# Kernel optimization log

Hardware: AMD Instinct MI355X
Metric: run time of the kernel (lower is better)

## Reference

```python
import jax, jax.numpy as jnp
import numpy as np

LENS = 0.4
DECAY = 0.2
THRESH = 0.2
LOG_SIG_MIN, LOG_SIG_MAX = -20.0, 2.0

# Surrogate-gradient spike: forward is heaviside, backward is rectangular window |x|<lens
@jax.custom_vjp
def act_fun(x):
    return (x > 0.0).astype(x.dtype)

def _act_fwd(x):
    return act_fun(x), x

def _act_bwd(x, g):
    return (g * (jnp.abs(x) < LENS).astype(g.dtype),)

act_fun.defvjp(_act_fwd, _act_bwd)


def _xavier(k, shape):
    fan_out, fan_in = shape
    lim = float(np.sqrt(6.0 / (fan_in + fan_out)))
    return jax.random.uniform(k, shape, jnp.float32, -lim, lim)


def setup_inputs() -> dict:
    key = jax.random.key(0)
    ks = jax.random.split(key, 9)
    B, IN, H, A = 4096, 512, 2048, 32
    return {
        "state": jax.random.normal(ks[0], (B, 5, IN), jnp.float32),
        "W_lif": _xavier(ks[1], (H, IN)), "b_lif": jnp.zeros((H,), jnp.float32),
        "W11": _xavier(ks[2], (H, H)), "b11": jnp.zeros((H,), jnp.float32),
        "W12": _xavier(ks[3], (H, H)), "b12": jnp.zeros((H,), jnp.float32),
        "W21": _xavier(ks[4], (H, H)), "b21": jnp.zeros((H,), jnp.float32),
        "W22": _xavier(ks[5], (H, H)), "b22": jnp.zeros((H,), jnp.float32),
        "Wm": _xavier(ks[6], (A, H)), "bm": jnp.zeros((A,), jnp.float32),
        "Wls": _xavier(ks[7], (A, H)), "bls": jnp.zeros((A,), jnp.float32),
    }


def reference(state, W_lif, b_lif, W11, b11, W12, b12, W21, b21, W22, b22, Wm, bm, Wls, bls):
    x_seq = jnp.repeat(state, 3, axis=1)
    # precompute fc(x) for all steps in one GEMM: [B,15,H]
    fc = jnp.einsum('bti,hi->bth', x_seq, W_lif) + b_lif
    B, T, H = fc.shape

    def step(carry, fc_t):
        mem, spike = carry
        mem1 = mem * DECAY * (1.0 - spike) + fc_t
        spike1 = act_fun(mem1 - THRESH)
        return (mem1, spike1), spike1

    init = (jnp.zeros((B, H), fc.dtype), jnp.zeros((B, H), fc.dtype))
    _, spikes = jax.lax.scan(step, init, jnp.swapaxes(fc, 0, 1))  # [T,B,H]
    x = jnp.mean(spikes, axis=0)  # [B,H]

    x1 = jax.nn.relu(x @ W11.T + b11)
    x1 = jax.nn.relu(x1 @ W12.T + b12)
    mean = x1 @ Wm.T + bm

    x2 = jax.nn.relu(x @ W21.T + b21)
    x2 = jax.nn.relu(x2 @ W22.T + b22)
    log_std = jnp.clip(x2 @ Wls.T + bls, LOG_SIG_MIN, LOG_SIG_MAX)
    return mean, log_std
```

## Files before the change

### kernel.cpp

```cpp
#include <hip/hip_runtime.h>
#include <hip/hip_bf16.h>


typedef _Float16 f16;
using f32x4 = __attribute__((ext_vector_type(4))) float;
using f16x8 = __attribute__((ext_vector_type(8))) f16;

#define MFMA16(a, b, c) __builtin_amdgcn_mfma_f32_16x16x32_f16((a), (b), (c), 0, 0, 0)
#define VMW8()  asm volatile("s_waitcnt vmcnt(8)" ::: "memory")
#define VMW4()  asm volatile("s_waitcnt vmcnt(4)" ::: "memory")
#define VMW0()  asm volatile("s_waitcnt vmcnt(0)" ::: "memory")
#define LGKM0() asm volatile("s_waitcnt lgkmcnt(0)" ::: "memory")
#define BARRIER() __builtin_amdgcn_s_barrier()
#define SCHED0() __builtin_amdgcn_sched_barrier(0)

__device__ __forceinline__ void gload16(const void* g, void* l) {
  __builtin_amdgcn_global_load_lds(
      (const __attribute__((address_space(1))) unsigned int*)g,
      (__attribute__((address_space(3))) unsigned int*)l, 16, 0, 0);
}

__device__ __forceinline__ void cvt8(const float4& a, const float4& b, f16* dst) {
  f16x8 d;
  d[0] = (f16)a.x; d[1] = (f16)a.y; d[2] = (f16)a.z; d[3] = (f16)a.w;
  d[4] = (f16)b.x; d[5] = (f16)b.y; d[6] = (f16)b.z; d[7] = (f16)b.w;
  *(f16x8*)dst = d;
}

__global__ __launch_bounds__(256) void cvt2b_kernel(
    const float* __restrict__ s0, f16* __restrict__ d0, int n8a,
    const float* __restrict__ s1, f16* __restrict__ d1, int n8b)
{
  int i = blockIdx.x * 256 + threadIdx.x;
  const float* src; f16* dst; int k;
  if (i < n8a) { src = s0; dst = d0; k = i; }
  else { k = i - n8a; if (k >= n8b) return; src = s1; dst = d1; }
  const float4* s4 = (const float4*)src;
  float4 a = s4[(size_t)k * 2], b = s4[(size_t)k * 2 + 1];
  cvt8(a, b, dst + (size_t)k * 8);
}

__global__ __launch_bounds__(256) void cvt4_kernel(
    const float* __restrict__ w0, const float* __restrict__ w1,
    const float* __restrict__ w2, const float* __restrict__ w3,
    f16* __restrict__ dst)
{
  int i = blockIdx.x * 256 + threadIdx.x;
  int which = i >> 19, k = i & 524287;
  const float* src = (which == 0) ? w0 : (which == 1) ? w1 : (which == 2) ? w2 : w3;
  const float4* s4 = (const float4*)src;
  float4 a = s4[(size_t)k * 2], b = s4[(size_t)k * 2 + 1];
  cvt8(a, b, dst + (size_t)i * 8);
}

__global__ __launch_bounds__(256) void cvt2_kernel(
    const float* __restrict__ s0, const float* __restrict__ s1,
    f16* __restrict__ d0, f16* __restrict__ d1, int n8each)
{
  int i = blockIdx.x * 256 + threadIdx.x;
  const float* src = (i < n8each) ? s0 : s1;
  f16* dst = (i < n8each) ? d0 : d1;
  int k = (i < n8each) ? i : i - n8each;
  if (k >= n8each) return;
  const float4* s4 = (const float4*)src;
  float4 a = s4[(size_t)k * 2], b = s4[(size_t)k * 2 + 1];
  cvt8(a, b, dst + (size_t)k * 8);
}

__global__ __launch_bounds__(512, 1) void lif256_kernel(
    const f16* __restrict__ S,
    const f16* __restrict__ W,
    const float* __restrict__ bl,
    f16* __restrict__ X)
{
  __shared__ alignas(16) f16 lds[4][128 * 64];

  const int tid = threadIdx.x, wid = tid >> 6, lane = tid & 63;
  const int wg = ((int)blockIdx.x % 8) * 64 + (int)blockIdx.x / 8;
  const int bn = wg & 15, bm = wg >> 4;
  const int b0 = bm * 128, h0 = bn * 128;
  const int wr0 = (wid >> 2) * 64, wc0 = (wid & 3) * 32;
  const int fr = lane & 15, fq = lane >> 4;
  const int sr = tid >> 3, scb = (tid & 7) * 16;

  f32x4 acc[4][2] = {};
  float mem[4][2][4] = {};
  float cnt[4][2][4] = {};

  char* Lb = (char*)&lds[0][0];
  const int xsw = (fr & 7) << 4;
  const int x0 = (fq * 16) ^ xsw;
  const int x1 = (64 + fq * 16) ^ xsw;
  char* const pA0 = Lb + (wr0 + fr) * 128 + x0;
  char* const pA1 = Lb + (wr0 + fr) * 128 + x1;
  char* const pB0 = Lb + 32768 + (wc0 + fr) * 128 + x0;
  char* const pB1 = Lb + 32768 + (wc0 + fr) * 128 + x1;

  const f16* sBase[2]; const f16* wBase[2];
#pragma unroll
  for (int l = 0; l < 2; ++l) {
    const int row = l * 64 + sr;
    const int c2 = scb ^ ((row & 7) << 4);
    sBase[l] = S + (size_t)(b0 + row) * 2560 + (c2 >> 1);
    wBase[l] = W + (size_t)(h0 + row) * 512 + (c2 >> 1);
  }

  auto STAGE = [&](int slot, int g) {
    const int koff = (g >> 3) * 512 + (g & 7) * 64;
    const int kw = (g & 7) * 64;
#pragma unroll
    for (int l = 0; l < 2; ++l)
      gload16(sBase[l] + koff, Lb + slot * 16384 + l * 8192 + tid * 16);
#pragma unroll
    for (int l = 0; l < 2; ++l)
      gload16(wBase[l] + kw, Lb + 32768 + slot * 16384 + l * 8192 + tid * 16);
  };

  const float bias[2] = { bl[h0 + wc0 + fr], bl[h0 + wc0 + 16 + fr] };

  STAGE(0, 0);
  STAGE(1, 1);
  VMW4();
  BARRIER();
  SCHED0();

#pragma unroll 2
  for (int g = 0; g < 40; ++g) {
    const int slot = g & 1;
    const int so = slot * 16384;

    f16x8 b[2][2], a[2][2];
#pragma unroll
    for (int nf = 0; nf < 2; ++nf) {
      b[nf][0] = *(const f16x8*)(pB0 + so + nf * 2048);
      b[nf][1] = *(const f16x8*)(pB1 + so + nf * 2048);
    }
#pragma unroll
    for (int i = 0; i < 2; ++i) {
      a[i][0] = *(const f16x8*)(pA0 + so + i * 2048);
      a[i][1] = *(const f16x8*)(pA1 + so + i * 2048);
    }
    BARRIER(); LGKM0(); SCHED0();
    __builtin_amdgcn_s_setprio(1);
#pragma unroll
    for (int i = 0; i < 2; ++i)
#pragma unroll
      for (int nf = 0; nf < 2; ++nf) {
        acc[i][nf] = MFMA16(a[i][0], b[nf][0], acc[i][nf]);
        acc[i][nf] = MFMA16(a[i][1], b[nf][1], acc[i][nf]);
      }
    __builtin_amdgcn_s_setprio(0);
    BARRIER();

#pragma unroll
    for (int i = 0; i < 2; ++i) {
      a[i][0] = *(const f16x8*)(pA0 + so + (2 + i) * 2048);
      a[i][1] = *(const f16x8*)(pA1 + so + (2 + i) * 2048);
    }
    LGKM0(); SCHED0();
    BARRIER();
    if (g + 2 < 40) STAGE(slot, g + 2);
    SCHED0();
    __builtin_amdgcn_s_setprio(1);
#pragma unroll
    for (int i = 0; i < 2; ++i)
#pragma unroll
      for (int nf = 0; nf < 2; ++nf) {
        acc[2 + i][nf] = MFMA16(a[i][0], b[nf][0], acc[2 + i][nf]);
        acc[2 + i][nf] = MFMA16(a[i][1], b[nf][1], acc[2 + i][nf]);
      }
    __builtin_amdgcn_s_setprio(0);

    if ((g & 7) == 7) {
#pragma unroll
      for (int mf = 0; mf < 4; ++mf)
#pragma unroll
        for (int nf = 0; nf < 2; ++nf) {
#pragma unroll
          for (int r = 0; r < 4; ++r) {
            const float fc = acc[mf][nf][r] + bias[nf];
            float m = mem[mf][nf][r], c = cnt[mf][nf][r];
#pragma unroll
            for (int j = 0; j < 3; ++j) {
              m = ((m > 0.2f) ? 0.f : m * 0.2f) + fc;
              c += (m > 0.2f) ? 1.f : 0.f;
            }
            mem[mf][nf][r] = m; cnt[mf][nf][r] = c;
          }
          acc[mf][nf] = f32x4{0.f, 0.f, 0.f, 0.f};
        }
    }

    if (g + 2 < 40)      { VMW4(); }
    else if (g + 1 < 40) { VMW0(); }
    BARRIER();
    SCHED0();
  }

#pragma unroll
  for (int nf = 0; nf < 2; ++nf) {
    const int col = h0 + wc0 + nf * 16 + fr;
#pragma unroll
    for (int mf = 0; mf < 4; ++mf) {
      const int row0 = b0 + wr0 + mf * 16 + fq * 4;
#pragma unroll
      for (int r = 0; r < 4; ++r)
        X[(size_t)(row0 + r) * 2048 + col] = (f16)(cnt[mf][nf][r] / 15.0f);
    }
  }
}

__global__ __launch_bounds__(512, 2) void trunk256_kernel(
    const f16* __restrict__ A0, const f16* __restrict__ A1, int lda,
    const f16* __restrict__ W0, const f16* __restrict__ W1,
    const float* __restrict__ bb0, const float* __restrict__ bb1,
    f16* __restrict__ C0, f16* __restrict__ C1, int ldc,
    int nbm, int nbn_half, int K)
{
  __shared__ alignas(16) f16 lds[4][256 * 64];

  const int tid = threadIdx.x, wid = tid >> 6, lane = tid & 63;
  const int nwg = nbm * nbn_half * 2, q8 = nwg / 8;
  const int wg = ((int)blockIdx.x % 8) * q8 + (int)blockIdx.x / 8;
  const int bmi = wg % nbm, t = wg / nbm;
  const int half = (t >= nbn_half);
  const f16* Ap = half ? A1 : A0;
  const f16* Wp = half ? W1 : W0;
  const float* bias = half ? bb1 : bb0;
  f16* C = half ? C1 : C0;
  const int bm0 = bmi * 256;
  const int bn0 = (half ? t - nbn_half : t) * 256;

  const int wr0 = (wid >> 2) * 128, wc0 = (wid & 3) * 64;
  const int fr = lane & 15, fq = lane >> 4;
  const int sr = tid >> 3, scb = (tid & 7) * 16;

  f32x4 acc[8][4] = {};
  const int NT = K / 64;

  char* Lb = (char*)&lds[0][0];
  const int xsw = (fr & 7) << 4;
  const int x0 = (fq * 16) ^ xsw;
  const int x1 = (64 + fq * 16) ^ xsw;
  char* const pA0 = Lb + (wr0 + fr) * 128 + x0;
  char* const pA1 = Lb + (wr0 + fr) * 128 + x1;
  char* const pB0 = Lb + 65536 + (wc0 + fr) * 128 + x0;
  char* const pB1 = Lb + 65536 + (wc0 + fr) * 128 + x1;

  const f16* aBase[4]; const f16* wBase[4];
#pragma unroll
  for (int l = 0; l < 4; ++l) {
    const int row = l * 64 + sr;
    const int c2 = scb ^ ((row & 7) << 4);
    aBase[l] = Ap + (size_t)(bm0 + row) * lda + (c2 >> 1);
    wBase[l] = Wp + (size_t)(bn0 + row) * K + (c2 >> 1);
  }

  auto STAGE = [&](int slot, int kt) {
    const int koff = kt * 64;
#pragma unroll
    for (int l = 0; l < 4; ++l)
      gload16(aBase[l] + koff, Lb + slot * 32768 + l * 8192 + tid * 16);
#pragma unroll
    for (int l = 0; l < 4; ++l)
      gload16(wBase[l] + koff, Lb + 65536 + slot * 32768 + l * 8192 + tid * 16);
  };

  STAGE(0, 0);
  STAGE(1, 1);
  VMW8();
  BARRIER();
  SCHED0();

#pragma unroll 2
  for (int kt = 0; kt < NT; ++kt) {
    const int slot = kt & 1;
    const int so = slot * 32768;

    f16x8 b[4][2];
#pragma unroll
    for (int nf = 0; nf < 4; ++nf) {
      b[nf][0] = *(const f16x8*)(pB0 + so + nf * 2048);
      b[nf][1] = *(const f16x8*)(pB1 + so + nf * 2048);
    }
    f16x8 a0[2][2], a1[2][2];
#pragma unroll
    for (int i = 0; i < 2; ++i) {
      a0[i][0] = *(const f16x8*)(pA0 + so + i * 2048);
      a0[i][1] = *(const f16x8*)(pA1 + so + i * 2048);
    }

    auto QUAD = [&](int mbase, f16x8 (&a)[2][2]) {
      __builtin_amdgcn_s_setprio(1);
#pragma unroll
      for (int nf = 0; nf < 4; ++nf) {
        acc[mbase][nf]     = MFMA16(a[0][0], b[nf][0], acc[mbase][nf]);
        acc[mbase][nf]     = MFMA16(a[0][1], b[nf][1], acc[mbase][nf]);
        acc[mbase + 1][nf] = MFMA16(a[1][0], b[nf][0], acc[mbase + 1][nf]);
        acc[mbase + 1][nf] = MFMA16(a[1][1], b[nf][1], acc[mbase + 1][nf]);
      }
      __builtin_amdgcn_s_setprio(0);
    };

#pragma unroll
    for (int i = 0; i < 2; ++i) {
      a1[i][0] = *(const f16x8*)(pA0 + so + (2 + i) * 2048);
      a1[i][1] = *(const f16x8*)(pA1 + so + (2 + i) * 2048);
    }
    QUAD(0, a0);
#pragma unroll
    for (int i = 0; i < 2; ++i) {
      a0[i][0] = *(const f16x8*)(pA0 + so + (4 + i) * 2048);
      a0[i][1] = *(const f16x8*)(pA1 + so + (4 + i) * 2048);
    }
    QUAD(2, a1);
#pragma unroll
    for (int i = 0; i < 2; ++i) {
      a1[i][0] = *(const f16x8*)(pA0 + so + (6 + i) * 2048);
      a1[i][1] = *(const f16x8*)(pA1 + so + (6 + i) * 2048);
    }
    QUAD(4, a0);
    QUAD(6, a1);

    LGKM0();
    BARRIER();
    SCHED0();
    if (kt + 2 < NT) {
      STAGE(slot, kt + 2);
      SCHED0();
      VMW8();
    } else if (kt + 1 < NT) {
      VMW0();
    }
    BARRIER();
    SCHED0();
  }

#pragma unroll
  for (int nf = 0; nf < 4; ++nf) {
    const int col = bn0 + wc0 + nf * 16 + fr;
    const float bv = bias[col];
#pragma unroll
    for (int m = 0; m < 8; ++m) {
      const int row0 = bm0 + wr0 + m * 16 + fq * 4;
#pragma unroll
      for (int r = 0; r < 4; ++r) {
        float v = fmaxf(acc[m][nf][r] + bv, 0.f);
        C[(size_t)(row0 + r) * ldc + col] = (f16)v;
      }
    }
  }
}

__global__ __launch_bounds__(256) void head_kernel(
    const f16* __restrict__ H1, const f16* __restrict__ H2,
    const f16* __restrict__ Wm, const float* __restrict__ bm,
    const f16* __restrict__ Wls, const float* __restrict__ bls,
    float* __restrict__ OUT, int M, int K)
{
  const int tid = threadIdx.x, wid = tid >> 6, lane = tid & 63;
  const int m0 = blockIdx.x * 64 + wid * 16;
  const int kb = (lane >> 4) * 8, fr = lane & 15, fq = lane >> 4;

  f32x4 a1[2] = {}, a2[2] = {};
  for (int k0 = 0; k0 < K; k0 += 32) {
    f16x8 f1 = *(const f16x8*)&H1[(size_t)(m0 + fr) * K + k0 + kb];
    f16x8 f2 = *(const f16x8*)&H2[(size_t)(m0 + fr) * K + k0 + kb];
#pragma unroll
    for (int n = 0; n < 2; ++n) {
      f16x8 wm = *(const f16x8*)&Wm[(size_t)(n * 16 + fr) * K + k0 + kb];
      f16x8 wl = *(const f16x8*)&Wls[(size_t)(n * 16 + fr) * K + k0 + kb];
      a1[n] = MFMA16(f1, wm, a1[n]);
      a2[n] = MFMA16(f2, wl, a2[n]);
    }
  }

#pragma unroll
  for (int n = 0; n < 2; ++n) {
    const int col = n * 16 + fr;
    const float bvm = bm[col];
    const float bvl = bls[col];
#pragma unroll
    for (int r = 0; r < 4; ++r) {
      const int row = m0 + fq * 4 + r;
      OUT[(size_t)row * 32 + col] = a1[n][r] + bvm;
      float lv = a2[n][r] + bvl;
      OUT[(size_t)M * 32 + (size_t)row * 32 + col] = fminf(fmaxf(lv, -20.f), 2.f);
    }
  }
}

extern "C" void kernel_launch(void* const* d_in, const int* in_sizes, int n_in,
                              void* d_out, int out_size, void* d_ws, size_t ws_size,
                              hipStream_t stream) {
  const float* state = (const float*)d_in[0];
  const float* W_lif = (const float*)d_in[1];
  const float* b_lif = (const float*)d_in[2];
  const float* W11   = (const float*)d_in[3];
  const float* b11   = (const float*)d_in[4];
  const float* W12   = (const float*)d_in[5];
  const float* b12   = (const float*)d_in[6];
  const float* W21   = (const float*)d_in[7];
  const float* b21   = (const float*)d_in[8];
  const float* W22   = (const float*)d_in[9];
  const float* b22   = (const float*)d_in[10];
  const float* Wm    = (const float*)d_in[11];
  const float* bm    = (const float*)d_in[12];
  const float* Wls   = (const float*)d_in[13];
  const float* bls   = (const float*)d_in[14];
  float* out = (float*)d_out;

  const int B = 4096, IN = 512, H = 2048;
  char* ws = (char*)d_ws;
  f16* x    = (f16*)(ws);
  f16* h1   = (f16*)(ws + 16777216);
  f16* h2   = (f16*)(ws + 33554432);
  f16* s16  = (f16*)(ws + 50331648);
  f16* wl16 = (f16*)(ws + 71303168);
  f16* w4   = (f16*)(ws + 50331648);
  f16* w11h = (f16*)(ws + 50331648);
  f16* w21h = (f16*)(ws + 58720256);
  f16* w12h = (f16*)(ws + 67108864);
  f16* w22h = (f16*)(ws + 75497472);
  f16* h22  = (f16*)(ws + 50331648);
  f16* wmh  = (f16*)(ws + 67108864);
  f16* wlsh = (f16*)(ws + 67239936);
  f16* h12  = x;

  const int n8s = B * 5 * IN / 8, n8w = H * IN / 8;
  cvt2b_kernel<<<(n8s + n8w + 255) / 256, 256, 0, stream>>>(
      state, s16, n8s, W_lif, wl16, n8w);

  lif256_kernel<<<512, 512, 0, stream>>>(s16, wl16, b_lif, x);

  cvt4_kernel<<<4 * 524288 / 256, 256, 0, stream>>>(W11, W21, W12, W22, w4);

  trunk256_kernel<<<256, 512, 0, stream>>>(x, x, H, w11h, w21h, b11, b21,
                                           h1, h2, H, 16, 8, H);
  trunk256_kernel<<<256, 512, 0, stream>>>(h1, h2, H, w12h, w22h, b12, b22,
                                           h12, h22, H, 16, 8, H);

  cvt2_kernel<<<2 * (32 * H / 8) / 256, 256, 0, stream>>>(Wm, Wls, wmh, wlsh, 32 * H / 8);
  head_kernel<<<B / 64, 256, 0, stream>>>(h12, h22, wmh, bm, wlsh, bls, out, B, H);
}
```

Baseline: 278.0 us.

## Triple-buffer LDS in LIF GEMM kernel to cut barriers per iteration

The LIF GEMM kernel moves from two LDS stages to three, so the prefetch for step g+2 can be issued at the top of each iteration into a slot not being read. All A fragments are now loaded at once, and the MFMAs run without the intermediate barriers, leaving one barrier per K-step. This removes synchronisation stalls and lets global loads overlap more compute. The cost is more LDS (96KB), more live registers for the extra A fragments, and runtime slot-rotation arithmetic in place of the unrolled-by-2 loop.

```diff
diff --git a/kernel.cpp b/kernel.cpp
--- a/kernel.cpp
+++ b/kernel.cpp
@@ -73,7 +73,7 @@
     const float* __restrict__ bl,
     f16* __restrict__ X)
 {
-  __shared__ alignas(16) f16 lds[4][128 * 64];
+  __shared__ alignas(16) f16 lds[6][128 * 64];
 
   const int tid = threadIdx.x, wid = tid >> 6, lane = tid & 63;
   const int wg = ((int)blockIdx.x % 8) * 64 + (int)blockIdx.x / 8;
@@ -93,8 +93,8 @@
   const int x1 = (64 + fq * 16) ^ xsw;
   char* const pA0 = Lb + (wr0 + fr) * 128 + x0;
   char* const pA1 = Lb + (wr0 + fr) * 128 + x1;
-  char* const pB0 = Lb + 32768 + (wc0 + fr) * 128 + x0;
-  char* const pB1 = Lb + 32768 + (wc0 + fr) * 128 + x1;
+  char* const pB0 = Lb + 49152 + (wc0 + fr) * 128 + x0;
+  char* const pB1 = Lb + 49152 + (wc0 + fr) * 128 + x1;
 
   const f16* sBase[2]; const f16* wBase[2];
 #pragma unroll
@@ -105,69 +105,58 @@
     wBase[l] = W + (size_t)(h0 + row) * 512 + (c2 >> 1);
   }
 
-  auto STAGE = [&](int slot, int g) {
+  auto STAGE = [&](int soSt, int g) {
     const int koff = (g >> 3) * 512 + (g & 7) * 64;
     const int kw = (g & 7) * 64;
 #pragma unroll
     for (int l = 0; l < 2; ++l)
-      gload16(sBase[l] + koff, Lb + slot * 16384 + l * 8192 + tid * 16);
+      gload16(sBase[l] + koff, Lb + soSt + l * 8192 + tid * 16);
 #pragma unroll
     for (int l = 0; l < 2; ++l)
-      gload16(wBase[l] + kw, Lb + 32768 + slot * 16384 + l * 8192 + tid * 16);
+      gload16(wBase[l] + kw, Lb + 49152 + soSt + l * 8192 + tid * 16);
   };
 
   const float bias[2] = { bl[h0 + wc0 + fr], bl[h0 + wc0 + 16 + fr] };
 
   STAGE(0, 0);
-  STAGE(1, 1);
+  STAGE(16384, 1);
   VMW4();
   BARRIER();
   SCHED0();
 
-#pragma unroll 2
+  int soRead = 0, soStage = 32768;
   for (int g = 0; g < 40; ++g) {
-    const int slot = g & 1;
-    const int so = slot * 16384;
-
-    f16x8 b[2][2], a[2][2];
+    if (g + 2 < 40) STAGE(soStage, g + 2);
+    SCHED0();
+
+    f16x8 b[2][2], a0[2][2], a1[2][2];
 #pragma unroll
     for (int nf = 0; nf < 2; ++nf) {
-      b[nf][0] = *(const f16x8*)(pB0 + so + nf * 2048);
-      b[nf][1] = *(const f16x8*)(pB1 + so + nf * 2048);
+      b[nf][0] = *(const f16x8*)(pB0 + soRead + nf * 2048);
+      b[nf][1] = *(const f16x8*)(pB1 + soRead + nf * 2048);
     }
 #pragma unroll
     for (int i = 0; i < 2; ++i) {
-      a[i][0] = *(const f16x8*)(pA0 + so + i * 2048);
-      a[i][1] = *(const f16x8*)(pA1 + so + i * 2048);
-    }
-    BARRIER(); LGKM0(); SCHED0();
+      a0[i][0] = *(const f16x8*)(pA0 + soRead + i * 2048);
+      a0[i][1] = *(const f16x8*)(pA1 + soRead + i * 2048);
+      a1[i][0] = *(const f16x8*)(pA0 + soRead + (2 + i) * 2048);
+      a1[i][1] = *(const f16x8*)(pA1 + soRead + (2 + i) * 2048);
+    }
+
     __builtin_amdgcn_s_setprio(1);
 #pragma unroll
     for (int i = 0; i < 2; ++i)
 #pragma unroll
       for (int nf = 0; nf < 2; ++nf) {
-        acc[i][nf] = MFMA16(a[i][0], b[nf][0], acc[i][nf]);
-        acc[i][nf] = MFMA16(a[i][1], b[nf][1], acc[i][nf]);
+        acc[i][nf] = MFMA16(a0[i][0], b[nf][0], acc[i][nf]);
+        acc[i][nf] = MFMA16(a0[i][1], b[nf][1], acc[i][nf]);
       }
-    __builtin_amdgcn_s_setprio(0);
-    BARRIER();
-
-#pragma unroll
-    for (int i = 0; i < 2; ++i) {
-      a[i][0] = *(const f16x8*)(pA0 + so + (2 + i) * 2048);
-      a[i][1] = *(const f16x8*)(pA1 + so + (2 + i) * 2048);
-    }
-    LGKM0(); SCHED0();
-    BARRIER();
-    if (g + 2 < 40) STAGE(slot, g + 2);
-    SCHED0();
-    __builtin_amdgcn_s_setprio(1);
 #pragma unroll
     for (int i = 0; i < 2; ++i)
 #pragma unroll
       for (int nf = 0; nf < 2; ++nf) {
-        acc[2 + i][nf] = MFMA16(a[i][0], b[nf][0], acc[2 + i][nf]);
-        acc[2 + i][nf] = MFMA16(a[i][1], b[nf][1], acc[2 + i][nf]);
+        acc[2 + i][nf] = MFMA16(a1[i][0], b[nf][0], acc[2 + i][nf]);
+        acc[2 + i][nf] = MFMA16(a1[i][1], b[nf][1], acc[2 + i][nf]);
       }
     __builtin_amdgcn_s_setprio(0);
 
@@ -191,10 +180,14 @@
         }
     }
 
+    LGKM0();
     if (g + 2 < 40)      { VMW4(); }
     else if (g + 1 < 40) { VMW0(); }
     BARRIER();
     SCHED0();
+
+    soRead  = (soRead  == 32768) ? 0 : soRead  + 16384;
+    soStage = (soStage == 32768) ? 0 : soStage + 16384;
   }
 
 #pragma unroll
```

Measured after the change: 269.2 us. 1.03x faster.
